# Performance work log

Measured on AMD Instinct MI355X. Metric: run time of the kernel, lower is better.

Reference implementation:

```python
import jax, jax.numpy as jnp
import numpy as np
from jax import lax

N = 2_097_152  # grid length
WENO5_MULT_BIAS = 0.1


def _conv1d(x, w, b, pad):
    # x: [1, C_in, L], w: [C_out, C_in, K] -> [1, C_out, L]
    y = lax.conv_general_dilated(x, w, window_strides=(1,), padding=[(pad, pad)],
                                 dimension_numbers=('NCH', 'OIH', 'NCH'))
    return y + b[None, :, None]


def _inner_nn_weno5(dif, w1, b1, w2, b2, w3, b3, w4, b4, w5, b5, w6, b6):
    # dif: [N] -> multiplier signal [N] in (0,1) via sigmoid
    x = dif[None, None, :]
    x = jax.nn.elu(_conv1d(x, w1, b1, 2))
    x = jax.nn.elu(_conv1d(x, w2, b2, 2))
    x = jax.nn.elu(_conv1d(x, w3, b3, 0))
    x = jax.nn.elu(_conv1d(x, w4, b4, 0))
    x = jax.nn.elu(_conv1d(x, w5, b5, 1))
    x = jax.nn.sigmoid(_conv1d(x, w6, b6, 0))
    return x[0, 0, :]


def _avg_diff(uu):
    # centered average of forward differences, replicated at the edges -> [N]
    dif = uu[1:] - uu[:-1]
    dif_left = jnp.concatenate([dif, dif[-1:]])
    dif_right = jnp.concatenate([dif[:1], dif])
    return 0.5 * dif_left + 0.5 * dif_right


def _fluxes_minus(u):
    f0 = (11 * u[3:-2] - 7 * u[4:-1] + 2 * u[5:]) / 6
    f1 = (2 * u[2:-3] + 5 * u[3:-2] - u[4:-1]) / 6
    f2 = (-u[1:-4] + 5 * u[2:-3] + 2 * u[3:-2]) / 6
    return f0, f1, f2


def _betas_minus(u):
    b0 = 13 / 12 * (u[3:-2] - 2 * u[4:-1] + u[5:]) ** 2 + 1 / 4 * (3 * u[3:-2] - 4 * u[4:-1] + u[5:]) ** 2
    b1 = 13 / 12 * (u[2:-3] - 2 * u[3:-2] + u[4:-1]) ** 2 + 1 / 4 * (u[2:-3] - u[4:-1]) ** 2
    b2 = 13 / 12 * (u[1:-4] - 2 * u[2:-3] + u[3:-2]) ** 2 + 1 / 4 * (u[1:-4] - 4 * u[2:-3] + 3 * u[3:-2]) ** 2
    return b0, b1, b2


def _weno5(uu, e, beta_mult):
    # w5_minus=True, mweno=True, mapped=False, trainable=True branch
    ur = uu[1:]
    ul = uu[:-1]
    fp = _fluxes_minus(ur)
    fn = _fluxes_minus(ul)
    bp = _betas_minus(ur)
    bn = _betas_minus(ul)
    # multipliers bm[3+shift:-3+shift] for shift in {-1,0,1}
    mul = (beta_mult[2:-4], beta_mult[3:-3], beta_mult[4:-2])
    bp = [b * m for b, m in zip(bp, mul)]
    bn = [b * m for b, m in zip(bn, mul)]
    ds = (1 / 10, 6 / 10, 3 / 10)

    def omegas_mweno(bs):
        brs = (bs[2] - bs[0]) ** 2
        o = [d / (e + b) ** 2 * (brs + (e + b) ** 2) for b, d in zip(bs, ds)]
        s = o[0] + o[1] + o[2]
        return [x / s for x in o]

    op = omegas_mweno(bp)
    on = omegas_mweno(bn)
    fluxp = op[0] * fp[0] + op[1] * fp[1] + op[2] * fp[2]
    fluxn = on[0] * fn[0] + on[1] * fn[1] + on[2] * fn[2]
    return fluxp - fluxn  # [N-6]


def setup_inputs() -> dict:
    key = jax.random.key(0)
    ks = jax.random.split(key, 14)
    uu = jax.random.normal(ks[0], (N,), dtype=jnp.float32)
    e = jnp.float32(1e-6)
    s = 0.1  # weight scale for stability
    w1 = s * jax.random.normal(ks[1], (20, 1, 5), jnp.float32)
    b1 = s * jax.random.normal(ks[2], (20,), jnp.float32)
    w2 = s * jax.random.normal(ks[3], (40, 20, 5), jnp.float32)
    b2 = s * jax.random.normal(ks[4], (40,), jnp.float32)
    w3 = s * jax.random.normal(ks[5], (80, 40, 1), jnp.float32)
    b3 = s * jax.random.normal(ks[6], (80,), jnp.float32)
    w4 = s * jax.random.normal(ks[7], (40, 80, 1), jnp.float32)
    b4 = s * jax.random.normal(ks[8], (40,), jnp.float32)
    w5 = s * jax.random.normal(ks[9], (20, 40, 3), jnp.float32)
    b5 = s * jax.random.normal(ks[10], (20,), jnp.float32)
    w6 = s * jax.random.normal(ks[11], (1, 20, 1), jnp.float32)
    b6 = s * jax.random.normal(ks[12], (1,), jnp.float32)
    return {"uu": uu, "e": e, "w1": w1, "b1": b1, "w2": w2, "b2": b2,
            "w3": w3, "b3": b3, "w4": w4, "b4": b4, "w5": w5, "b5": b5,
            "w6": w6, "b6": b6}


def reference(uu, e, w1, b1, w2, b2, w3, b3, w4, b4, w5, b5, w6, b6):
    dif = _avg_diff(uu)
    beta_mult = _inner_nn_weno5(dif, w1, b1, w2, b2, w3, b3, w4, b4, w5, b5, w6, b6) + WENO5_MULT_BIAS
    return _weno5(uu, e, beta_mult)
```

## Files before the change

### kernel.cpp

```cpp
#include <hip/hip_runtime.h>
#include <math.h>

#define NTHREADS 512
#define TOUT 252
#define NP 256
#define X1ROWS 260
#define X1S 40
#define X2S 40
#define T3S 80
#define X4S 40
#define X5S 26
#define NDIF 264
#define NUU 266

#define F2_BASE 0
#define F3_BASE 15
#define F4_BASE 25
#define F5_BASE 34
#define NFRAGS 42

typedef unsigned short u16;
typedef unsigned int u32;
typedef __attribute__((ext_vector_type(8))) short bf16x8;
typedef __attribute__((ext_vector_type(4))) float f32x4;

__device__ __forceinline__ float elu_f(float x) {
    return x > 0.0f ? x : (__expf(x) - 1.0f);
}
__device__ __forceinline__ float sq_f(float x) { return x * x; }
__device__ __forceinline__ u16 f2bf(float f) {
    union { float f; u32 u; } v; v.f = f;
    u32 r = v.u + 0x7FFFu + ((v.u >> 16) & 1u);
    return (u16)(r >> 16);
}
__device__ __forceinline__ float bf2f(u16 h) {
    union { u32 u; float f; } v; v.u = ((u32)h) << 16;
    return v.f;
}
__device__ __forceinline__ u32 pack_trunc(float a, float b) {
    union { float f; u32 u; } va, vb; va.f = a; vb.f = b;
#if __has_builtin(__builtin_amdgcn_perm)
    return __builtin_amdgcn_perm(vb.u, va.u, 0x07060302u);
#else
    return (vb.u & 0xFFFF0000u) | (va.u >> 16);
#endif
}

__global__ __launch_bounds__(64) void build_frags_kernel(
    const float* __restrict__ w2, const float* __restrict__ w3,
    const float* __restrict__ w4, const float* __restrict__ w5,
    u16* __restrict__ ws)
{
    const int f = blockIdx.x;
    const int lane = threadIdx.x;
    const int m = lane & 15;
    const int q = lane >> 4;
    float wvv[8];
    #pragma unroll
    for (int j = 0; j < 8; ++j) wvv[j] = 0.0f;

    if (f < F3_BASE) {
        int mt = (f - F2_BASE) / 5, s = (f - F2_BASE) % 5;
        int oc = mt * 16 + m;
        #pragma unroll
        for (int j = 0; j < 8; ++j) {
            int ic = q * 8 + j;
            if (oc < 40 && ic < 20) wvv[j] = w2[oc * 100 + ic * 5 + s];
        }
    } else if (f < F4_BASE) {
        int mt = (f - F3_BASE) / 2, s = (f - F3_BASE) % 2;
        int oc = mt * 16 + m;
        #pragma unroll
        for (int j = 0; j < 8; ++j) {
            int k = s * 32 + q * 8 + j;
            if (k < 40) wvv[j] = w3[oc * 40 + k];
        }
    } else if (f < F5_BASE) {
        int mt = (f - F4_BASE) / 3, s = (f - F4_BASE) % 3;
        int oc = mt * 16 + m;
        #pragma unroll
        for (int j = 0; j < 8; ++j) {
            int k = s * 32 + q * 8 + j;
            if (oc < 40 && k < 80) wvv[j] = w4[oc * 80 + k];
        }
    } else {
        int mt = (f - F5_BASE) / 4, s = (f - F5_BASE) % 4;
        int oc = mt * 16 + m;
        int k0 = s * 32 + q * 8;
        int dk = k0 / 40, ic0 = k0 - dk * 40;
        #pragma unroll
        for (int j = 0; j < 8; ++j) {
            if (oc < 20 && k0 < 120) wvv[j] = w5[oc * 120 + (ic0 + j) * 3 + dk];
        }
    }
    u32 pk[4];
    #pragma unroll
    for (int p = 0; p < 4; ++p)
        pk[p] = (u32)f2bf(wvv[2 * p]) | ((u32)f2bf(wvv[2 * p + 1]) << 16);
    u32* wp = (u32*)&ws[(f * 64 + lane) * 8];
    wp[0] = pk[0]; wp[1] = pk[1]; wp[2] = pk[2]; wp[3] = pk[3];
}

__device__ __forceinline__ bf16x8 ld_frag(const u16* ws, int f, int lane) {
    return *(const bf16x8*)&ws[(f * 64 + lane) * 8];
}

__global__ __launch_bounds__(NTHREADS, 1) void weno_nn_kernel(
    const float* __restrict__ uu, const float* __restrict__ e_ptr,
    const float* __restrict__ w1, const float* __restrict__ b1,
    const float* __restrict__ b2, const float* __restrict__ b3,
    const float* __restrict__ b4, const float* __restrict__ b5,
    const float* __restrict__ w6, const float* __restrict__ b6,
    const u16* __restrict__ wfr,
    float* __restrict__ out, int n_out, int N)
{
    __shared__ float s_uu[NUU];
    __shared__ float s_dif[NDIF];
    __shared__ __align__(16) u16 bufA[NP * T3S];
    __shared__ __align__(16) u16 bufB[258 * X4S];

    const int tid  = threadIdx.x;
    const int lane = tid & 63;
    const int wv_id = __builtin_amdgcn_readfirstlane(tid >> 6);
    const int m    = lane & 15;
    const int q    = lane >> 4;
    const int J0   = blockIdx.x * TOUT;
    const int P0   = J0 + 2;
    const int U0   = J0 - 4;

    for (int i = tid; i < NUU; i += NTHREADS) {
        int g = U0 + i;
        s_uu[i] = (g >= 0 && g < N) ? uu[g] : 0.0f;
    }
    __syncthreads();

    for (int d = tid; d < NDIF; d += NTHREADS) {
        int g = P0 - 5 + d;
        float v = 0.0f;
        if (g >= 0 && g < N) {
            int j1 = g < N - 2 ? g : N - 2;
            int j0 = g - 1 > 0 ? g - 1 : 0;
            float dl = s_uu[j1 + 1 - U0] - s_uu[j1 - U0];
            float dr = s_uu[j0 + 1 - U0] - s_uu[j0 - U0];
            v = 0.5f * (dl + dr);
        }
        s_dif[d] = v;
    }
    __syncthreads();

    for (int s = tid; s < X1ROWS; s += NTHREADS) {
        int g = P0 - 3 + s;
        bool valid = (g >= 0 && g < N);
        float dv[5];
        #pragma unroll
        for (int k = 0; k < 5; ++k) dv[k] = s_dif[s + k];
        float v[20];
        #pragma unroll
        for (int oc = 0; oc < 20; ++oc) {
            float a = b1[oc];
            #pragma unroll
            for (int k = 0; k < 5; ++k) a += w1[oc * 5 + k] * dv[k];
            v[oc] = valid ? elu_f(a) : 0.0f;
        }
        u32* rp = (u32*)&bufA[s * X1S];
        #pragma unroll
        for (int p = 0; p < 10; ++p)
            rp[p] = pack_trunc(v[2 * p], v[2 * p + 1]);
        #pragma unroll
        for (int p = 10; p < 16; ++p) rp[p] = 0;
    }
    __syncthreads();

    {
        bf16x8 a2[3][5];
        #pragma unroll
        for (int mt = 0; mt < 3; ++mt)
            #pragma unroll
            for (int s = 0; s < 5; ++s)
                a2[mt][s] = ld_frag(wfr, F2_BASE + mt * 5 + s, lane);
        f32x4 bias2[3];
        #pragma unroll
        for (int mt = 0; mt < 3; ++mt) {
            #pragma unroll
            for (int r = 0; r < 4; ++r) {
                int oc = mt * 16 + 4 * q + r;
                bias2[mt][r] = (oc < 40) ? b2[oc] : 0.0f;
            }
        }
        for (int t = 0; t < 2; ++t) {
            const int N0 = (wv_id * 2 + t) * 16;
            f32x4 acc[3];
            #pragma unroll
            for (int mt = 0; mt < 3; ++mt) acc[mt] = bias2[mt];
            #pragma unroll
            for (int s = 0; s < 5; ++s) {
                bf16x8 bfrag = *(const bf16x8*)&bufA[(N0 + m + s) * X1S + q * 8];
                #pragma unroll
                for (int mt = 0; mt < 3; ++mt)
                    acc[mt] = __builtin_amdgcn_mfma_f32_16x16x32_bf16(a2[mt][s], bfrag, acc[mt], 0, 0, 0);
            }
            #pragma unroll
            for (int mt = 0; mt < 3; ++mt) {
                int oc0 = mt * 16 + 4 * q;
                if (oc0 < 40) {
                    u32* wp = (u32*)&bufB[(N0 + m) * X2S + oc0];
                    wp[0] = pack_trunc(elu_f(acc[mt][0]), elu_f(acc[mt][1]));
                    wp[1] = pack_trunc(elu_f(acc[mt][2]), elu_f(acc[mt][3]));
                }
            }
        }
    }
    __syncthreads();

    {
        bf16x8 a3[5][2];
        #pragma unroll
        for (int mt = 0; mt < 5; ++mt)
            #pragma unroll
            for (int s = 0; s < 2; ++s)
                a3[mt][s] = ld_frag(wfr, F3_BASE + mt * 2 + s, lane);
        f32x4 bias3[5];
        #pragma unroll
        for (int mt = 0; mt < 5; ++mt) {
            #pragma unroll
            for (int r = 0; r < 4; ++r) bias3[mt][r] = b3[mt * 16 + 4 * q + r];
        }
        for (int t = 0; t < 2; ++t) {
            const int N0 = (wv_id * 2 + t) * 16;
            f32x4 acc[5];
            #pragma unroll
            for (int mt = 0; mt < 5; ++mt) acc[mt] = bias3[mt];
            {
                bf16x8 bfrag = *(const bf16x8*)&bufB[(N0 + m) * X2S + q * 8];
                #pragma unroll
                for (int mt = 0; mt < 5; ++mt)
                    acc[mt] = __builtin_amdgcn_mfma_f32_16x16x32_bf16(a3[mt][0], bfrag, acc[mt], 0, 0, 0);
            }
            {
                bf16x8 bfrag = *(const bf16x8*)&bufB[(N0 + m) * X2S + ((q == 0) ? 32 : 0)];
                #pragma unroll
                for (int mt = 0; mt < 5; ++mt)
                    acc[mt] = __builtin_amdgcn_mfma_f32_16x16x32_bf16(a3[mt][1], bfrag, acc[mt], 0, 0, 0);
            }
            #pragma unroll
            for (int mt = 0; mt < 5; ++mt) {
                int oc0 = mt * 16 + 4 * q;
                u32* wp = (u32*)&bufA[(N0 + m) * T3S + oc0];
                wp[0] = pack_trunc(elu_f(acc[mt][0]), elu_f(acc[mt][1]));
                wp[1] = pack_trunc(elu_f(acc[mt][2]), elu_f(acc[mt][3]));
            }
        }
    }
    __syncthreads();

    {
        bf16x8 a4[3][3];
        #pragma unroll
        for (int mt = 0; mt < 3; ++mt)
            #pragma unroll
            for (int s = 0; s < 3; ++s)
                a4[mt][s] = ld_frag(wfr, F4_BASE + mt * 3 + s, lane);
        f32x4 bias4[3];
        #pragma unroll
        for (int mt = 0; mt < 3; ++mt) {
            #pragma unroll
            for (int r = 0; r < 4; ++r) {
                int oc = mt * 16 + 4 * q + r;
                bias4[mt][r] = (oc < 40) ? b4[oc] : 0.0f;
            }
        }
        if (tid < 80) bufB[256 * X4S + tid] = 0;
        for (int t = 0; t < 2; ++t) {
            const int N0 = (wv_id * 2 + t) * 16;
            f32x4 acc[3];
            #pragma unroll
            for (int mt = 0; mt < 3; ++mt) acc[mt] = bias4[mt];
            #pragma unroll
            for (int s = 0; s < 3; ++s) {
                int k0 = s * 32 + q * 8;
                bf16x8 bfrag = *(const bf16x8*)&bufA[(N0 + m) * T3S + ((k0 < 80) ? k0 : 0)];
                #pragma unroll
                for (int mt = 0; mt < 3; ++mt)
                    acc[mt] = __builtin_amdgcn_mfma_f32_16x16x32_bf16(a4[mt][s], bfrag, acc[mt], 0, 0, 0);
            }
            #pragma unroll
            for (int mt = 0; mt < 3; ++mt) {
                int oc0 = mt * 16 + 4 * q;
                if (oc0 < 40) {
                    u32* wp = (u32*)&bufB[(N0 + m) * X4S + oc0];
                    wp[0] = pack_trunc(elu_f(acc[mt][0]), elu_f(acc[mt][1]));
                    wp[1] = pack_trunc(elu_f(acc[mt][2]), elu_f(acc[mt][3]));
                }
            }
        }
    }
    __syncthreads();

    {
        bf16x8 a5[2][4];
        #pragma unroll
        for (int mt = 0; mt < 2; ++mt)
            #pragma unroll
            for (int s = 0; s < 4; ++s)
                a5[mt][s] = ld_frag(wfr, F5_BASE + mt * 4 + s, lane);
        f32x4 bias5[2];
        #pragma unroll
        for (int mt = 0; mt < 2; ++mt) {
            #pragma unroll
            for (int r = 0; r < 4; ++r) {
                int oc = mt * 16 + 4 * q + r;
                bias5[mt][r] = (oc < 20) ? b5[oc] : 0.0f;
            }
        }
        for (int t = 0; t < 2; ++t) {
            const int N0 = (wv_id * 2 + t) * 16;
            f32x4 acc[2];
            #pragma unroll
            for (int mt = 0; mt < 2; ++mt) acc[mt] = bias5[mt];
            #pragma unroll
            for (int s = 0; s < 4; ++s) {
                int k0 = s * 32 + q * 8;
                int dk = (k0 < 120) ? (k0 / 40) : 0;
                int ic0 = (k0 < 120) ? (k0 - dk * 40) : 0;
                bf16x8 bfrag = *(const bf16x8*)&bufB[(N0 + m + dk) * X4S + ic0];
                #pragma unroll
                for (int mt = 0; mt < 2; ++mt)
                    acc[mt] = __builtin_amdgcn_mfma_f32_16x16x32_bf16(a5[mt][s], bfrag, acc[mt], 0, 0, 0);
            }
            #pragma unroll
            for (int mt = 0; mt < 2; ++mt) {
                int oc0 = mt * 16 + 4 * q;
                if (oc0 < 20) {
                    u32* wp = (u32*)&bufA[(N0 + m) * X5S + oc0];
                    wp[0] = pack_trunc(elu_f(acc[mt][0]), elu_f(acc[mt][1]));
                    wp[1] = pack_trunc(elu_f(acc[mt][2]), elu_f(acc[mt][3]));
                }
            }
        }
    }
    __syncthreads();

    if (tid < 254) {
        float a = b6[0];
        #pragma unroll
        for (int c = 0; c < 20; ++c)
            a += w6[c] * bf2f(bufA[tid * X5S + c]);
        s_dif[tid] = 1.0f / (1.0f + __expf(-a)) + 0.1f;
    }
    __syncthreads();

    const float eps = e_ptr[0];
    if (tid < TOUT) {
        int j = J0 + tid;
        if (j < n_out) {
            float a  = s_uu[tid + 5];
            float b  = s_uu[tid + 6];
            float c  = s_uu[tid + 7];
            float d  = s_uu[tid + 8];
            float ee = s_uu[tid + 9];
            float f  = s_uu[tid + 10];
            float m0 = s_dif[tid];
            float m1 = s_dif[tid + 1];
            float m2 = s_dif[tid + 2];

            const float i6 = 1.0f / 6.0f;
            float fp0 = (11.f * d - 7.f * ee + 2.f * f) * i6;
            float fp1 = (2.f * c + 5.f * d - ee) * i6;
            float fp2 = (-b + 5.f * c + 2.f * d) * i6;
            float fn0 = (11.f * c - 7.f * d + 2.f * ee) * i6;
            float fn1 = (2.f * b + 5.f * c - d) * i6;
            float fn2 = (-a + 5.f * b + 2.f * c) * i6;

            const float c1312 = 13.f / 12.f;
            float bp0 = c1312 * sq_f(d - 2.f * ee + f) + 0.25f * sq_f(3.f * d - 4.f * ee + f);
            float bp1 = c1312 * sq_f(c - 2.f * d + ee) + 0.25f * sq_f(c - ee);
            float bp2 = c1312 * sq_f(b - 2.f * c + d) + 0.25f * sq_f(b - 4.f * c + 3.f * d);
            float bn0 = c1312 * sq_f(c - 2.f * d + ee) + 0.25f * sq_f(3.f * c - 4.f * d + ee);
            float bn1 = c1312 * sq_f(b - 2.f * c + d) + 0.25f * sq_f(b - d);
            float bn2 = c1312 * sq_f(a - 2.f * b + c) + 0.25f * sq_f(a - 4.f * b + 3.f * c);

            bp0 *= m0; bp1 *= m1; bp2 *= m2;
            bn0 *= m0; bn1 *= m1; bn2 *= m2;

            float q0 = eps + bp0; q0 *= q0;
            float q1 = eps + bp1; q1 *= q1;
            float q2 = eps + bp2; q2 *= q2;
            float brs = bp2 - bp0; brs *= brs;
            float o0 = 0.1f * (1.f + brs / q0);
            float o1 = 0.6f * (1.f + brs / q1);
            float o2 = 0.3f * (1.f + brs / q2);
            float inv = 1.f / (o0 + o1 + o2);
            float fluxp = (o0 * fp0 + o1 * fp1 + o2 * fp2) * inv;

            q0 = eps + bn0; q0 *= q0;
            q1 = eps + bn1; q1 *= q1;
            q2 = eps + bn2; q2 *= q2;
            brs = bn2 - bn0; brs *= brs;
            o0 = 0.1f * (1.f + brs / q0);
            o1 = 0.6f * (1.f + brs / q1);
            o2 = 0.3f * (1.f + brs / q2);
            inv = 1.f / (o0 + o1 + o2);
            float fluxn = (o0 * fn0 + o1 * fn1 + o2 * fn2) * inv;

            out[j] = fluxp - fluxn;
        }
    }
}

extern "C" void kernel_launch(void* const* d_in, const int* in_sizes, int n_in,
                              void* d_out, int out_size, void* d_ws, size_t ws_size,
                              hipStream_t stream) {
    const float* uu = (const float*)d_in[0];
    const float* e  = (const float*)d_in[1];
    const float* w1 = (const float*)d_in[2];
    const float* b1 = (const float*)d_in[3];
    const float* w2 = (const float*)d_in[4];
    const float* b2 = (const float*)d_in[5];
    const float* w3 = (const float*)d_in[6];
    const float* b3 = (const float*)d_in[7];
    const float* w4 = (const float*)d_in[8];
    const float* b4 = (const float*)d_in[9];
    const float* w5 = (const float*)d_in[10];
    const float* b5 = (const float*)d_in[11];
    const float* w6 = (const float*)d_in[12];
    const float* b6 = (const float*)d_in[13];
    float* out = (float*)d_out;
    u16* wfr = (u16*)d_ws;
    const int N = in_sizes[0];
    const int nblocks = (out_size + TOUT - 1) / TOUT;

    build_frags_kernel<<<NFRAGS, 64, 0, stream>>>(w2, w3, w4, w5, wfr);
    weno_nn_kernel<<<nblocks, NTHREADS, 0, stream>>>(
        uu, e, w1, b1, b2, b3, b4, b5, w6, b6, wfr,
        out, out_size, N);
}
```

Measured before the change: 286.4 us.

## Fuse conv layers 2-4 per wave, fold biases into GEMM, shrink LDS for occupancy

Layers 2, 3 and 4 now run back-to-back within each wave on its own rows. Layer 3 output is streamed in 32-channel chunks straight into layer 4's accumulation, which removes two block-wide barriers and the full 80-channel intermediate buffer. The biases for layers 2 and 4 are folded into the weight fragments via a constant-one input column. Weight fragments are loaded on demand instead of kept in registers, LDS is repacked into a smaller aliased buffer, and launch bounds are raised to allow more resident blocks per CU. The trade-off is repeated weight loads from global/L1, plus reliance on compiler fences for intra-wave LDS ordering.

```diff
diff --git a/kernel.cpp b/kernel.cpp
--- a/kernel.cpp
+++ b/kernel.cpp
@@ -3,15 +3,19 @@
 
 #define NTHREADS 512
 #define TOUT 252
-#define NP 256
-#define X1ROWS 260
-#define X1S 40
-#define X2S 40
-#define T3S 80
-#define X4S 40
-#define X5S 26
 #define NDIF 264
 #define NUU 266
+
+#define X1S 24
+#define X2S 40
+#define T3S 32
+#define X5S 24
+
+#define SUU_OFF  0
+#define X1_OFF   1072
+#define T3_OFF   13600
+#define BUFB_OFF 29984
+#define SMEM_SIZE 50624
 
 #define F2_BASE 0
 #define F3_BASE 15
@@ -23,6 +27,8 @@
 typedef unsigned int u32;
 typedef __attribute__((ext_vector_type(8))) short bf16x8;
 typedef __attribute__((ext_vector_type(4))) float f32x4;
+
+#define MEM_FENCE() __asm__ __volatile__("" ::: "memory")
 
 __device__ __forceinline__ float elu_f(float x) {
     return x > 0.0f ? x : (__expf(x) - 1.0f);
@@ -47,8 +53,10 @@
 }
 
 __global__ __launch_bounds__(64) void build_frags_kernel(
-    const float* __restrict__ w2, const float* __restrict__ w3,
-    const float* __restrict__ w4, const float* __restrict__ w5,
+    const float* __restrict__ w2, const float* __restrict__ b2,
+    const float* __restrict__ w3,
+    const float* __restrict__ w4, const float* __restrict__ b4,
+    const float* __restrict__ w5,
     u16* __restrict__ ws)
 {
     const int f = blockIdx.x;
@@ -67,6 +75,7 @@
             int ic = q * 8 + j;
             if (oc < 40 && ic < 20) wvv[j] = w2[oc * 100 + ic * 5 + s];
         }
+        if (s == 2 && q == 2 && oc < 40) wvv[4] = b2[oc];
     } else if (f < F4_BASE) {
         int mt = (f - F3_BASE) / 2, s = (f - F3_BASE) % 2;
         int oc = mt * 16 + m;
@@ -83,6 +92,7 @@
             int k = s * 32 + q * 8 + j;
             if (oc < 40 && k < 80) wvv[j] = w4[oc * 80 + k];
         }
+        if (s == 2 && q == 2 && oc < 40) wvv[0] = b4[oc];
     } else {
         int mt = (f - F5_BASE) / 4, s = (f - F5_BASE) % 4;
         int oc = mt * 16 + m;
@@ -105,23 +115,26 @@
     return *(const bf16x8*)&ws[(f * 64 + lane) * 8];
 }
 
-__global__ __launch_bounds__(NTHREADS, 1) void weno_nn_kernel(
+__global__ __launch_bounds__(NTHREADS, 6) void weno_nn_kernel(
     const float* __restrict__ uu, const float* __restrict__ e_ptr,
     const float* __restrict__ w1, const float* __restrict__ b1,
-    const float* __restrict__ b2, const float* __restrict__ b3,
-    const float* __restrict__ b4, const float* __restrict__ b5,
+    const float* __restrict__ b3, const float* __restrict__ b5,
     const float* __restrict__ w6, const float* __restrict__ b6,
     const u16* __restrict__ wfr,
     float* __restrict__ out, int n_out, int N)
 {
-    __shared__ float s_uu[NUU];
-    __shared__ float s_dif[NDIF];
-    __shared__ __align__(16) u16 bufA[NP * T3S];
-    __shared__ __align__(16) u16 bufB[258 * X4S];
+    __shared__ __align__(16) unsigned char smem[SMEM_SIZE];
+    float* s_uu  = (float*)(smem + SUU_OFF);
+    float* s_dif = (float*)(smem + T3_OFF);
+    u16*   x1    = (u16*)(smem + X1_OFF);
+    u16*   x5    = (u16*)(smem + X1_OFF);
+    u16*   t3    = (u16*)(smem + T3_OFF);
+    u16*   xB    = (u16*)(smem + BUFB_OFF);
+    float* beta  = (float*)(smem + BUFB_OFF);
 
     const int tid  = threadIdx.x;
     const int lane = tid & 63;
-    const int wv_id = __builtin_amdgcn_readfirstlane(tid >> 6);
+    const int wv   = __builtin_amdgcn_readfirstlane(tid >> 6);
     const int m    = lane & 15;
     const int q    = lane >> 4;
     const int J0   = blockIdx.x * TOUT;
@@ -148,7 +161,9 @@
     }
     __syncthreads();
 
-    for (int s = tid; s < X1ROWS; s += NTHREADS) {
+    if (tid < 40) ((u32*)&xB[256 * X2S])[tid] = 0;
+    if (tid >= 64 && tid < 76) ((u32*)&x1[260 * X1S])[tid - 64] = 0;
+    for (int s = tid; s < 260; s += NTHREADS) {
         int g = P0 - 3 + s;
         bool valid = (g >= 0 && g < N);
         float dv[5];
@@ -162,179 +177,108 @@
             for (int k = 0; k < 5; ++k) a += w1[oc * 5 + k] * dv[k];
             v[oc] = valid ? elu_f(a) : 0.0f;
         }
-        u32* rp = (u32*)&bufA[s * X1S];
+        u32* rp = (u32*)&x1[s * X1S];
         #pragma unroll
         for (int p = 0; p < 10; ++p)
             rp[p] = pack_trunc(v[2 * p], v[2 * p + 1]);
-        #pragma unroll
-        for (int p = 10; p < 16; ++p) rp[p] = 0;
-    }
-    __syncthreads();
-
-    {
-        bf16x8 a2[3][5];
-        #pragma unroll
-        for (int mt = 0; mt < 3; ++mt)
+        rp[10] = valid ? 0x00003F80u : 0u;
+        rp[11] = 0u;
+    }
+    __syncthreads();
+
+    for (int t = 0; t < 2; ++t) {
+        const int row = (wv * 2 + t) * 16 + m;
+
+        bf16x8 Bx1[5];
+        #pragma unroll
+        for (int s = 0; s < 5; ++s)
+            Bx1[s] = *(const bf16x8*)&x1[(row + s) * X1S + q * 8];
+        #pragma unroll
+        for (int mt2 = 0; mt2 < 3; ++mt2) {
+            f32x4 acc = {0.f, 0.f, 0.f, 0.f};
             #pragma unroll
             for (int s = 0; s < 5; ++s)
-                a2[mt][s] = ld_frag(wfr, F2_BASE + mt * 5 + s, lane);
-        f32x4 bias2[3];
-        #pragma unroll
-        for (int mt = 0; mt < 3; ++mt) {
-            #pragma unroll
-            for (int r = 0; r < 4; ++r) {
-                int oc = mt * 16 + 4 * q + r;
-                bias2[mt][r] = (oc < 40) ? b2[oc] : 0.0f;
+                acc = __builtin_amdgcn_mfma_f32_16x16x32_bf16(
+                    ld_frag(wfr, F2_BASE + mt2 * 5 + s, lane), Bx1[s], acc, 0, 0, 0);
+            int oc0 = mt2 * 16 + 4 * q;
+            if (oc0 < 40) {
+                u32* wp = (u32*)&xB[row * X2S + oc0];
+                wp[0] = pack_trunc(elu_f(acc[0]), elu_f(acc[1]));
+                wp[1] = pack_trunc(elu_f(acc[2]), elu_f(acc[3]));
             }
         }
-        for (int t = 0; t < 2; ++t) {
-            const int N0 = (wv_id * 2 + t) * 16;
-            f32x4 acc[3];
-            #pragma unroll
-            for (int mt = 0; mt < 3; ++mt) acc[mt] = bias2[mt];
-            #pragma unroll
-            for (int s = 0; s < 5; ++s) {
-                bf16x8 bfrag = *(const bf16x8*)&bufA[(N0 + m + s) * X1S + q * 8];
-                #pragma unroll
-                for (int mt = 0; mt < 3; ++mt)
-                    acc[mt] = __builtin_amdgcn_mfma_f32_16x16x32_bf16(a2[mt][s], bfrag, acc[mt], 0, 0, 0);
+        MEM_FENCE();
+
+        bf16x8 Bx2a = *(const bf16x8*)&xB[row * X2S + q * 8];
+        bf16x8 Bx2b = *(const bf16x8*)&xB[row * X2S + ((q == 0) ? 32 : 0)];
+        f32x4 acc4[3];
+        #pragma unroll
+        for (int mt4 = 0; mt4 < 3; ++mt4)
+            acc4[mt4] = (f32x4){0.f, 0.f, 0.f, 0.f};
+        #pragma unroll
+        for (int p3 = 0; p3 < 3; ++p3) {
+            const int nmt = (p3 < 2) ? 2 : 1;
+            #pragma unroll
+            for (int i = 0; i < nmt; ++i) {
+                int mt = 2 * p3 + i;
+                f32x4 a3 = *(const f32x4*)&b3[16 * mt + 4 * q];
+                a3 = __builtin_amdgcn_mfma_f32_16x16x32_bf16(
+                    ld_frag(wfr, F3_BASE + mt * 2 + 0, lane), Bx2a, a3, 0, 0, 0);
+                a3 = __builtin_amdgcn_mfma_f32_16x16x32_bf16(
+                    ld_frag(wfr, F3_BASE + mt * 2 + 1, lane), Bx2b, a3, 0, 0, 0);
+                u32* wp = (u32*)&t3[row * T3S + 16 * i + 4 * q];
+                wp[0] = pack_trunc(elu_f(a3[0]), elu_f(a3[1]));
+                wp[1] = pack_trunc(elu_f(a3[2]), elu_f(a3[3]));
             }
-            #pragma unroll
-            for (int mt = 0; mt < 3; ++mt) {
-                int oc0 = mt * 16 + 4 * q;
-                if (oc0 < 40) {
-                    u32* wp = (u32*)&bufB[(N0 + m) * X2S + oc0];
-                    wp[0] = pack_trunc(elu_f(acc[mt][0]), elu_f(acc[mt][1]));
-                    wp[1] = pack_trunc(elu_f(acc[mt][2]), elu_f(acc[mt][3]));
-                }
+            if (p3 == 2 && q == 0)
+                *(u32*)&t3[row * T3S + 16] = 0x00003F80u;
+            MEM_FENCE();
+            bf16x8 Bt = *(const bf16x8*)&t3[row * T3S + q * 8];
+            #pragma unroll
+            for (int mt4 = 0; mt4 < 3; ++mt4)
+                acc4[mt4] = __builtin_amdgcn_mfma_f32_16x16x32_bf16(
+                    ld_frag(wfr, F4_BASE + mt4 * 3 + p3, lane), Bt, acc4[mt4], 0, 0, 0);
+            MEM_FENCE();
+        }
+        #pragma unroll
+        for (int mt4 = 0; mt4 < 3; ++mt4) {
+            int oc0 = mt4 * 16 + 4 * q;
+            if (oc0 < 40) {
+                u32* wp = (u32*)&xB[row * X2S + oc0];
+                wp[0] = pack_trunc(elu_f(acc4[mt4][0]), elu_f(acc4[mt4][1]));
+                wp[1] = pack_trunc(elu_f(acc4[mt4][2]), elu_f(acc4[mt4][3]));
             }
         }
-    }
-    __syncthreads();
-
-    {
-        bf16x8 a3[5][2];
-        #pragma unroll
-        for (int mt = 0; mt < 5; ++mt)
-            #pragma unroll
-            for (int s = 0; s < 2; ++s)
-                a3[mt][s] = ld_frag(wfr, F3_BASE + mt * 2 + s, lane);
-        f32x4 bias3[5];
-        #pragma unroll
-        for (int mt = 0; mt < 5; ++mt) {
-            #pragma unroll
-            for (int r = 0; r < 4; ++r) bias3[mt][r] = b3[mt * 16 + 4 * q + r];
-        }
-        for (int t = 0; t < 2; ++t) {
-            const int N0 = (wv_id * 2 + t) * 16;
-            f32x4 acc[5];
-            #pragma unroll
-            for (int mt = 0; mt < 5; ++mt) acc[mt] = bias3[mt];
-            {
-                bf16x8 bfrag = *(const bf16x8*)&bufB[(N0 + m) * X2S + q * 8];
-                #pragma unroll
-                for (int mt = 0; mt < 5; ++mt)
-                    acc[mt] = __builtin_amdgcn_mfma_f32_16x16x32_bf16(a3[mt][0], bfrag, acc[mt], 0, 0, 0);
-            }
-            {
-                bf16x8 bfrag = *(const bf16x8*)&bufB[(N0 + m) * X2S + ((q == 0) ? 32 : 0)];
-                #pragma unroll
-                for (int mt = 0; mt < 5; ++mt)
-                    acc[mt] = __builtin_amdgcn_mfma_f32_16x16x32_bf16(a3[mt][1], bfrag, acc[mt], 0, 0, 0);
-            }
-            #pragma unroll
-            for (int mt = 0; mt < 5; ++mt) {
-                int oc0 = mt * 16 + 4 * q;
-                u32* wp = (u32*)&bufA[(N0 + m) * T3S + oc0];
-                wp[0] = pack_trunc(elu_f(acc[mt][0]), elu_f(acc[mt][1]));
-                wp[1] = pack_trunc(elu_f(acc[mt][2]), elu_f(acc[mt][3]));
-            }
-        }
-    }
-    __syncthreads();
-
-    {
-        bf16x8 a4[3][3];
-        #pragma unroll
-        for (int mt = 0; mt < 3; ++mt)
-            #pragma unroll
-            for (int s = 0; s < 3; ++s)
-                a4[mt][s] = ld_frag(wfr, F4_BASE + mt * 3 + s, lane);
-        f32x4 bias4[3];
-        #pragma unroll
-        for (int mt = 0; mt < 3; ++mt) {
-            #pragma unroll
-            for (int r = 0; r < 4; ++r) {
-                int oc = mt * 16 + 4 * q + r;
-                bias4[mt][r] = (oc < 40) ? b4[oc] : 0.0f;
-            }
-        }
-        if (tid < 80) bufB[256 * X4S + tid] = 0;
-        for (int t = 0; t < 2; ++t) {
-            const int N0 = (wv_id * 2 + t) * 16;
-            f32x4 acc[3];
-            #pragma unroll
-            for (int mt = 0; mt < 3; ++mt) acc[mt] = bias4[mt];
-            #pragma unroll
-            for (int s = 0; s < 3; ++s) {
-                int k0 = s * 32 + q * 8;
-                bf16x8 bfrag = *(const bf16x8*)&bufA[(N0 + m) * T3S + ((k0 < 80) ? k0 : 0)];
-                #pragma unroll
-                for (int mt = 0; mt < 3; ++mt)
-                    acc[mt] = __builtin_amdgcn_mfma_f32_16x16x32_bf16(a4[mt][s], bfrag, acc[mt], 0, 0, 0);
-            }
-            #pragma unroll
-            for (int mt = 0; mt < 3; ++mt) {
-                int oc0 = mt * 16 + 4 * q;
-                if (oc0 < 40) {
-                    u32* wp = (u32*)&bufB[(N0 + m) * X4S + oc0];
-                    wp[0] = pack_trunc(elu_f(acc[mt][0]), elu_f(acc[mt][1]));
-                    wp[1] = pack_trunc(elu_f(acc[mt][2]), elu_f(acc[mt][3]));
-                }
-            }
-        }
-    }
-    __syncthreads();
-
-    {
-        bf16x8 a5[2][4];
-        #pragma unroll
-        for (int mt = 0; mt < 2; ++mt)
+        MEM_FENCE();
+    }
+    __syncthreads();
+
+    for (int t = 0; t < 2; ++t) {
+        const int row = (wv * 2 + t) * 16 + m;
+        bf16x8 B5[4];
+        #pragma unroll
+        for (int s = 0; s < 4; ++s) {
+            int k0 = 32 * s + 8 * q;
+            int dk, ic0;
+            if (k0 < 120) {
+                dk = (k0 >= 80) ? 2 : ((k0 >= 40) ? 1 : 0);
+                ic0 = k0 - 40 * dk;
+            } else { dk = 0; ic0 = 0; }
+            B5[s] = *(const bf16x8*)&xB[(row + dk) * X2S + ic0];
+        }
+        #pragma unroll
+        for (int mt5 = 0; mt5 < 2; ++mt5) {
+            int bo = (mt5 == 0) ? 4 * q : 16;
+            f32x4 acc = *(const f32x4*)&b5[bo];
             #pragma unroll
             for (int s = 0; s < 4; ++s)
-                a5[mt][s] = ld_frag(wfr, F5_BASE + mt * 4 + s, lane);
-        f32x4 bias5[2];
-        #pragma unroll
-        for (int mt = 0; mt < 2; ++mt) {
-            #pragma unroll
-            for (int r = 0; r < 4; ++r) {
-                int oc = mt * 16 + 4 * q + r;
-                bias5[mt][r] = (oc < 20) ? b5[oc] : 0.0f;
-            }
-        }
-        for (int t = 0; t < 2; ++t) {
-            const int N0 = (wv_id * 2 + t) * 16;
-            f32x4 acc[2];
-            #pragma unroll
-            for (int mt = 0; mt < 2; ++mt) acc[mt] = bias5[mt];
-            #pragma unroll
-            for (int s = 0; s < 4; ++s) {
-                int k0 = s * 32 + q * 8;
-                int dk = (k0 < 120) ? (k0 / 40) : 0;
-                int ic0 = (k0 < 120) ? (k0 - dk * 40) : 0;
-                bf16x8 bfrag = *(const bf16x8*)&bufB[(N0 + m + dk) * X4S + ic0];
-                #pragma unroll
-                for (int mt = 0; mt < 2; ++mt)
-                    acc[mt] = __builtin_amdgcn_mfma_f32_16x16x32_bf16(a5[mt][s], bfrag, acc[mt], 0, 0, 0);
-            }
-            #pragma unroll
-            for (int mt = 0; mt < 2; ++mt) {
-                int oc0 = mt * 16 + 4 * q;
-                if (oc0 < 20) {
-                    u32* wp = (u32*)&bufA[(N0 + m) * X5S + oc0];
-                    wp[0] = pack_trunc(elu_f(acc[mt][0]), elu_f(acc[mt][1]));
-                    wp[1] = pack_trunc(elu_f(acc[mt][2]), elu_f(acc[mt][3]));
-                }
+                acc = __builtin_amdgcn_mfma_f32_16x16x32_bf16(
+                    ld_frag(wfr, F5_BASE + mt5 * 4 + s, lane), B5[s], acc, 0, 0, 0);
+            int oc0 = mt5 * 16 + 4 * q;
+            if (oc0 < 20) {
+                u32* wp = (u32*)&x5[row * X5S + oc0];
+                wp[0] = pack_trunc(elu_f(acc[0]), elu_f(acc[1]));
+                wp[1] = pack_trunc(elu_f(acc[2]), elu_f(acc[3]));
             }
         }
     }
@@ -344,8 +288,8 @@
         float a = b6[0];
         #pragma unroll
         for (int c = 0; c < 20; ++c)
-            a += w6[c] * bf2f(bufA[tid * X5S + c]);
-        s_dif[tid] = 1.0f / (1.0f + __expf(-a)) + 0.1f;
+            a += w6[c] * bf2f(x5[tid * X5S + c]);
+        beta[tid] = 1.0f / (1.0f + __expf(-a)) + 0.1f;
     }
     __syncthreads();
 
@@ -359,9 +303,9 @@
             float d  = s_uu[tid + 8];
             float ee = s_uu[tid + 9];
             float f  = s_uu[tid + 10];
-            float m0 = s_dif[tid];
-            float m1 = s_dif[tid + 1];
-            float m2 = s_dif[tid + 2];
+            float m0 = beta[tid];
+            float m1 = beta[tid + 1];
+            float m2 = beta[tid + 2];
 
             const float i6 = 1.0f / 6.0f;
             float fp0 = (11.f * d - 7.f * ee + 2.f * f) * i6;
@@ -429,8 +373,8 @@
     const int N = in_sizes[0];
     const int nblocks = (out_size + TOUT - 1) / TOUT;
 
-    build_frags_kernel<<<NFRAGS, 64, 0, stream>>>(w2, w3, w4, w5, wfr);
+    build_frags_kernel<<<NFRAGS, 64, 0, stream>>>(w2, b2, w3, w4, b4, w5, wfr);
     weno_nn_kernel<<<nblocks, NTHREADS, 0, stream>>>(
-        uu, e, w1, b1, b2, b3, b4, b5, w6, b6, wfr,
+        uu, e, w1, b1, b3, b5, w6, b6, wfr,
         out, out_size, N);
 }
```

Result: no change. 292.0 us (+2.0%).

## Split conv3 channels across passes to shrink shared memory and raise occupancy

Applied to the files above, without the earlier changes.

Conv3 output (80 channels) is split into two chunks (32 and 48 channels) that are each consumed by a partial conv4 accumulation, so the full 80-wide intermediate never sits in shared memory. Buffers are overlaid in one aliased byte array, cutting LDS from about 73KB to about 48KB, and the launch bound no longer forces one block per CU, so more blocks can share a CU. Weight fragments are loaded from global memory at each MFMA instead of being held in registers, which lowers register pressure but adds extra loads and two more barriers.

```diff
diff --git a/kernel.cpp b/kernel.cpp
--- a/kernel.cpp
+++ b/kernel.cpp
@@ -3,15 +3,20 @@
 
 #define NTHREADS 512
 #define TOUT 252
-#define NP 256
-#define X1ROWS 260
+#define NDIF 264
+#define NUU 266
+
 #define X1S 40
 #define X2S 40
-#define T3S 80
-#define X4S 40
+#define T3AS 34
+#define T3BS 50
 #define X5S 26
-#define NDIF 264
-#define NUU 266
+
+#define SUU_OFF  0
+#define SDIF_OFF 1072
+#define RA_OFF   2144
+#define RB_OFF   27744
+#define SMEM_SIZE 48384
 
 #define F2_BASE 0
 #define F3_BASE 15
@@ -33,9 +38,11 @@
     u32 r = v.u + 0x7FFFu + ((v.u >> 16) & 1u);
     return (u16)(r >> 16);
 }
-__device__ __forceinline__ float bf2f(u16 h) {
-    union { u32 u; float f; } v; v.u = ((u32)h) << 16;
-    return v.f;
+__device__ __forceinline__ float bf_lo(u32 u) {
+    union { u32 u; float f; } v; v.u = u << 16; return v.f;
+}
+__device__ __forceinline__ float bf_hi(u32 u) {
+    union { u32 u; float f; } v; v.u = u & 0xFFFF0000u; return v.f;
 }
 __device__ __forceinline__ u32 pack_trunc(float a, float b) {
     union { float f; u32 u; } va, vb; va.f = a; vb.f = b;
@@ -105,7 +112,7 @@
     return *(const bf16x8*)&ws[(f * 64 + lane) * 8];
 }
 
-__global__ __launch_bounds__(NTHREADS, 1) void weno_nn_kernel(
+__global__ __launch_bounds__(NTHREADS) void weno_nn_kernel(
     const float* __restrict__ uu, const float* __restrict__ e_ptr,
     const float* __restrict__ w1, const float* __restrict__ b1,
     const float* __restrict__ b2, const float* __restrict__ b3,
@@ -114,14 +121,19 @@
     const u16* __restrict__ wfr,
     float* __restrict__ out, int n_out, int N)
 {
-    __shared__ float s_uu[NUU];
-    __shared__ float s_dif[NDIF];
-    __shared__ __align__(16) u16 bufA[NP * T3S];
-    __shared__ __align__(16) u16 bufB[258 * X4S];
+    __shared__ __align__(16) unsigned char smem[SMEM_SIZE];
+    float* s_uu  = (float*)(smem + SUU_OFF);
+    float* s_dif = (float*)(smem + SDIF_OFF);
+    u16*   x1    = (u16*)(smem + RA_OFF);
+    u16*   t3a   = (u16*)(smem + RA_OFF);
+    u16*   t3b   = (u16*)(smem + RA_OFF);
+    u16*   x5    = (u16*)(smem + RA_OFF);
+    u16*   xB    = (u16*)(smem + RB_OFF);
+    float* beta  = (float*)(smem + RB_OFF);
 
     const int tid  = threadIdx.x;
     const int lane = tid & 63;
-    const int wv_id = __builtin_amdgcn_readfirstlane(tid >> 6);
+    const int wv   = __builtin_amdgcn_readfirstlane(tid >> 6);
     const int m    = lane & 15;
     const int q    = lane >> 4;
     const int J0   = blockIdx.x * TOUT;
@@ -148,7 +160,8 @@
     }
     __syncthreads();
 
-    for (int s = tid; s < X1ROWS; s += NTHREADS) {
+    if (tid < 40) ((u32*)&xB[256 * X2S])[tid] = 0;
+    for (int s = tid; s < 260; s += NTHREADS) {
         int g = P0 - 3 + s;
         bool valid = (g >= 0 && g < N);
         float dv[5];
@@ -162,7 +175,7 @@
             for (int k = 0; k < 5; ++k) a += w1[oc * 5 + k] * dv[k];
             v[oc] = valid ? elu_f(a) : 0.0f;
         }
-        u32* rp = (u32*)&bufA[s * X1S];
+        u32* rp = (u32*)&x1[s * X1S];
         #pragma unroll
         for (int p = 0; p < 10; ++p)
             rp[p] = pack_trunc(v[2 * p], v[2 * p + 1]);
@@ -188,13 +201,13 @@
             }
         }
         for (int t = 0; t < 2; ++t) {
-            const int N0 = (wv_id * 2 + t) * 16;
+            const int N0 = (wv * 2 + t) * 16;
             f32x4 acc[3];
             #pragma unroll
             for (int mt = 0; mt < 3; ++mt) acc[mt] = bias2[mt];
             #pragma unroll
             for (int s = 0; s < 5; ++s) {
-                bf16x8 bfrag = *(const bf16x8*)&bufA[(N0 + m + s) * X1S + q * 8];
+                bf16x8 bfrag = *(const bf16x8*)&x1[(N0 + m + s) * X1S + q * 8];
                 #pragma unroll
                 for (int mt = 0; mt < 3; ++mt)
                     acc[mt] = __builtin_amdgcn_mfma_f32_16x16x32_bf16(a2[mt][s], bfrag, acc[mt], 0, 0, 0);
@@ -203,7 +216,7 @@
             for (int mt = 0; mt < 3; ++mt) {
                 int oc0 = mt * 16 + 4 * q;
                 if (oc0 < 40) {
-                    u32* wp = (u32*)&bufB[(N0 + m) * X2S + oc0];
+                    u32* wp = (u32*)&xB[(N0 + m) * X2S + oc0];
                     wp[0] = pack_trunc(elu_f(acc[mt][0]), elu_f(acc[mt][1]));
                     wp[1] = pack_trunc(elu_f(acc[mt][2]), elu_f(acc[mt][3]));
                 }
@@ -212,140 +225,125 @@
     }
     __syncthreads();
 
-    {
-        bf16x8 a3[5][2];
-        #pragma unroll
-        for (int mt = 0; mt < 5; ++mt)
-            #pragma unroll
-            for (int s = 0; s < 2; ++s)
-                a3[mt][s] = ld_frag(wfr, F3_BASE + mt * 2 + s, lane);
-        f32x4 bias3[5];
-        #pragma unroll
-        for (int mt = 0; mt < 5; ++mt) {
-            #pragma unroll
-            for (int r = 0; r < 4; ++r) bias3[mt][r] = b3[mt * 16 + 4 * q + r];
-        }
-        for (int t = 0; t < 2; ++t) {
-            const int N0 = (wv_id * 2 + t) * 16;
-            f32x4 acc[5];
-            #pragma unroll
-            for (int mt = 0; mt < 5; ++mt) acc[mt] = bias3[mt];
-            {
-                bf16x8 bfrag = *(const bf16x8*)&bufB[(N0 + m) * X2S + q * 8];
-                #pragma unroll
-                for (int mt = 0; mt < 5; ++mt)
-                    acc[mt] = __builtin_amdgcn_mfma_f32_16x16x32_bf16(a3[mt][0], bfrag, acc[mt], 0, 0, 0);
-            }
-            {
-                bf16x8 bfrag = *(const bf16x8*)&bufB[(N0 + m) * X2S + ((q == 0) ? 32 : 0)];
-                #pragma unroll
-                for (int mt = 0; mt < 5; ++mt)
-                    acc[mt] = __builtin_amdgcn_mfma_f32_16x16x32_bf16(a3[mt][1], bfrag, acc[mt], 0, 0, 0);
-            }
-            #pragma unroll
-            for (int mt = 0; mt < 5; ++mt) {
-                int oc0 = mt * 16 + 4 * q;
-                u32* wp = (u32*)&bufA[(N0 + m) * T3S + oc0];
-                wp[0] = pack_trunc(elu_f(acc[mt][0]), elu_f(acc[mt][1]));
-                wp[1] = pack_trunc(elu_f(acc[mt][2]), elu_f(acc[mt][3]));
-            }
-        }
-    }
-    __syncthreads();
-
-    {
-        bf16x8 a4[3][3];
-        #pragma unroll
-        for (int mt = 0; mt < 3; ++mt)
-            #pragma unroll
-            for (int s = 0; s < 3; ++s)
-                a4[mt][s] = ld_frag(wfr, F4_BASE + mt * 3 + s, lane);
-        f32x4 bias4[3];
+    bf16x8 Bx2[2][2];
+    f32x4  acc4[2][3];
+    #pragma unroll
+    for (int t = 0; t < 2; ++t) {
         #pragma unroll
         for (int mt = 0; mt < 3; ++mt) {
             #pragma unroll
             for (int r = 0; r < 4; ++r) {
                 int oc = mt * 16 + 4 * q + r;
-                bias4[mt][r] = (oc < 40) ? b4[oc] : 0.0f;
-            }
-        }
-        if (tid < 80) bufB[256 * X4S + tid] = 0;
-        for (int t = 0; t < 2; ++t) {
-            const int N0 = (wv_id * 2 + t) * 16;
-            f32x4 acc[3];
-            #pragma unroll
-            for (int mt = 0; mt < 3; ++mt) acc[mt] = bias4[mt];
-            #pragma unroll
-            for (int s = 0; s < 3; ++s) {
-                int k0 = s * 32 + q * 8;
-                bf16x8 bfrag = *(const bf16x8*)&bufA[(N0 + m) * T3S + ((k0 < 80) ? k0 : 0)];
-                #pragma unroll
-                for (int mt = 0; mt < 3; ++mt)
-                    acc[mt] = __builtin_amdgcn_mfma_f32_16x16x32_bf16(a4[mt][s], bfrag, acc[mt], 0, 0, 0);
-            }
-            #pragma unroll
-            for (int mt = 0; mt < 3; ++mt) {
-                int oc0 = mt * 16 + 4 * q;
-                if (oc0 < 40) {
-                    u32* wp = (u32*)&bufB[(N0 + m) * X4S + oc0];
-                    wp[0] = pack_trunc(elu_f(acc[mt][0]), elu_f(acc[mt][1]));
-                    wp[1] = pack_trunc(elu_f(acc[mt][2]), elu_f(acc[mt][3]));
-                }
-            }
-        }
-    }
-    __syncthreads();
-
-    {
-        bf16x8 a5[2][4];
-        #pragma unroll
-        for (int mt = 0; mt < 2; ++mt)
-            #pragma unroll
-            for (int s = 0; s < 4; ++s)
-                a5[mt][s] = ld_frag(wfr, F5_BASE + mt * 4 + s, lane);
-        f32x4 bias5[2];
+                acc4[t][mt][r] = (oc < 40) ? b4[oc] : 0.0f;
+            }
+        }
+    }
+
+    for (int t = 0; t < 2; ++t) {
+        const int rowi = (wv * 2 + t) * 16 + m;
+        Bx2[t][0] = *(const bf16x8*)&xB[rowi * X2S + q * 8];
+        Bx2[t][1] = *(const bf16x8*)&xB[rowi * X2S + ((q == 0) ? 32 : 0)];
         #pragma unroll
         for (int mt = 0; mt < 2; ++mt) {
+            f32x4 a3;
+            #pragma unroll
+            for (int r = 0; r < 4; ++r) a3[r] = b3[mt * 16 + 4 * q + r];
+            a3 = __builtin_amdgcn_mfma_f32_16x16x32_bf16(ld_frag(wfr, F3_BASE + mt * 2 + 0, lane), Bx2[t][0], a3, 0, 0, 0);
+            a3 = __builtin_amdgcn_mfma_f32_16x16x32_bf16(ld_frag(wfr, F3_BASE + mt * 2 + 1, lane), Bx2[t][1], a3, 0, 0, 0);
+            u32* wp = (u32*)&t3a[rowi * T3AS + mt * 16 + 4 * q];
+            wp[0] = pack_trunc(elu_f(a3[0]), elu_f(a3[1]));
+            wp[1] = pack_trunc(elu_f(a3[2]), elu_f(a3[3]));
+        }
+    }
+    __syncthreads();
+
+    for (int t = 0; t < 2; ++t) {
+        const int rowi = (wv * 2 + t) * 16 + m;
+        bf16x8 Bt = *(const bf16x8*)&t3a[rowi * T3AS + q * 8];
+        #pragma unroll
+        for (int mt = 0; mt < 3; ++mt)
+            acc4[t][mt] = __builtin_amdgcn_mfma_f32_16x16x32_bf16(ld_frag(wfr, F4_BASE + mt * 3 + 0, lane), Bt, acc4[t][mt], 0, 0, 0);
+    }
+    __syncthreads();
+
+    for (int t = 0; t < 2; ++t) {
+        const int rowi = (wv * 2 + t) * 16 + m;
+        #pragma unroll
+        for (int mtb = 0; mtb < 3; ++mtb) {
+            const int mt = mtb + 2;
+            f32x4 a3;
+            #pragma unroll
+            for (int r = 0; r < 4; ++r) a3[r] = b3[mt * 16 + 4 * q + r];
+            a3 = __builtin_amdgcn_mfma_f32_16x16x32_bf16(ld_frag(wfr, F3_BASE + mt * 2 + 0, lane), Bx2[t][0], a3, 0, 0, 0);
+            a3 = __builtin_amdgcn_mfma_f32_16x16x32_bf16(ld_frag(wfr, F3_BASE + mt * 2 + 1, lane), Bx2[t][1], a3, 0, 0, 0);
+            u32* wp = (u32*)&t3b[rowi * T3BS + mtb * 16 + 4 * q];
+            wp[0] = pack_trunc(elu_f(a3[0]), elu_f(a3[1]));
+            wp[1] = pack_trunc(elu_f(a3[2]), elu_f(a3[3]));
+        }
+    }
+    __syncthreads();
+
+    for (int t = 0; t < 2; ++t) {
+        const int rowi = (wv * 2 + t) * 16 + m;
+        bf16x8 Bt1 = *(const bf16x8*)&t3b[rowi * T3BS + q * 8];
+        bf16x8 Bt2 = *(const bf16x8*)&t3b[rowi * T3BS + ((q < 2) ? (32 + q * 8) : 0)];
+        #pragma unroll
+        for (int mt = 0; mt < 3; ++mt) {
+            acc4[t][mt] = __builtin_amdgcn_mfma_f32_16x16x32_bf16(ld_frag(wfr, F4_BASE + mt * 3 + 1, lane), Bt1, acc4[t][mt], 0, 0, 0);
+            acc4[t][mt] = __builtin_amdgcn_mfma_f32_16x16x32_bf16(ld_frag(wfr, F4_BASE + mt * 3 + 2, lane), Bt2, acc4[t][mt], 0, 0, 0);
+            int oc0 = mt * 16 + 4 * q;
+            if (oc0 < 40) {
+                u32* wp = (u32*)&xB[rowi * X2S + oc0];
+                wp[0] = pack_trunc(elu_f(acc4[t][mt][0]), elu_f(acc4[t][mt][1]));
+                wp[1] = pack_trunc(elu_f(acc4[t][mt][2]), elu_f(acc4[t][mt][3]));
+            }
+        }
+    }
+    __syncthreads();
+
+    for (int t = 0; t < 2; ++t) {
+        const int rowi = (wv * 2 + t) * 16 + m;
+        bf16x8 B5[4];
+        #pragma unroll
+        for (int s = 0; s < 4; ++s) {
+            int k0 = 32 * s + 8 * q;
+            int dk, ic0;
+            if (k0 < 120) {
+                dk = (k0 >= 80) ? 2 : ((k0 >= 40) ? 1 : 0);
+                ic0 = k0 - 40 * dk;
+            } else { dk = 0; ic0 = 0; }
+            B5[s] = *(const bf16x8*)&xB[(rowi + dk) * X2S + ic0];
+        }
+        #pragma unroll
+        for (int mt = 0; mt < 2; ++mt) {
+            f32x4 acc;
             #pragma unroll
             for (int r = 0; r < 4; ++r) {
                 int oc = mt * 16 + 4 * q + r;
-                bias5[mt][r] = (oc < 20) ? b5[oc] : 0.0f;
-            }
-        }
-        for (int t = 0; t < 2; ++t) {
-            const int N0 = (wv_id * 2 + t) * 16;
-            f32x4 acc[2];
-            #pragma unroll
-            for (int mt = 0; mt < 2; ++mt) acc[mt] = bias5[mt];
-            #pragma unroll
-            for (int s = 0; s < 4; ++s) {
-                int k0 = s * 32 + q * 8;
-                int dk = (k0 < 120) ? (k0 / 40) : 0;
-                int ic0 = (k0 < 120) ? (k0 - dk * 40) : 0;
-                bf16x8 bfrag = *(const bf16x8*)&bufB[(N0 + m + dk) * X4S + ic0];
-                #pragma unroll
-                for (int mt = 0; mt < 2; ++mt)
-                    acc[mt] = __builtin_amdgcn_mfma_f32_16x16x32_bf16(a5[mt][s], bfrag, acc[mt], 0, 0, 0);
-            }
-            #pragma unroll
-            for (int mt = 0; mt < 2; ++mt) {
-                int oc0 = mt * 16 + 4 * q;
-                if (oc0 < 20) {
-                    u32* wp = (u32*)&bufA[(N0 + m) * X5S + oc0];
-                    wp[0] = pack_trunc(elu_f(acc[mt][0]), elu_f(acc[mt][1]));
-                    wp[1] = pack_trunc(elu_f(acc[mt][2]), elu_f(acc[mt][3]));
-                }
+                acc[r] = (oc < 20) ? b5[oc] : 0.0f;
+            }
+            #pragma unroll
+            for (int s = 0; s < 4; ++s)
+                acc = __builtin_amdgcn_mfma_f32_16x16x32_bf16(ld_frag(wfr, F5_BASE + mt * 4 + s, lane), B5[s], acc, 0, 0, 0);
+            int oc0 = mt * 16 + 4 * q;
+            if (oc0 < 20) {
+                u32* wp = (u32*)&x5[rowi * X5S + oc0];
+                wp[0] = pack_trunc(elu_f(acc[0]), elu_f(acc[1]));
+                wp[1] = pack_trunc(elu_f(acc[2]), elu_f(acc[3]));
             }
         }
     }
     __syncthreads();
 
     if (tid < 254) {
+        const u32* xp = (const u32*)&x5[tid * X5S];
         float a = b6[0];
         #pragma unroll
-        for (int c = 0; c < 20; ++c)
-            a += w6[c] * bf2f(bufA[tid * X5S + c]);
-        s_dif[tid] = 1.0f / (1.0f + __expf(-a)) + 0.1f;
+        for (int p = 0; p < 10; ++p) {
+            u32 u = xp[p];
+            a += w6[2 * p] * bf_lo(u) + w6[2 * p + 1] * bf_hi(u);
+        }
+        beta[tid] = 1.0f / (1.0f + __expf(-a)) + 0.1f;
     }
     __syncthreads();
 
@@ -359,9 +357,9 @@
             float d  = s_uu[tid + 8];
             float ee = s_uu[tid + 9];
             float f  = s_uu[tid + 10];
-            float m0 = s_dif[tid];
-            float m1 = s_dif[tid + 1];
-            float m2 = s_dif[tid + 2];
+            float m0 = beta[tid];
+            float m1 = beta[tid + 1];
+            float m2 = beta[tid + 2];
 
             const float i6 = 1.0f / 6.0f;
             float fp0 = (11.f * d - 7.f * ee + 2.f * f) * i6;
```

Result: slower. 313.4 us (+9.4%).
